# Optimization experiments

Measured on AMD Instinct MI355X. Metric: run time of the kernel, lower is better.

Reference implementation:

```python
import jax, jax.numpy as jnp
import numpy as np

B, S, DIM, H = 2, 2048, 1024, 16
HD = DIM // H  # 64


def setup_inputs() -> dict:
    key = jax.random.key(0)
    ks = jax.random.split(key, 7)
    sc = 1.0 / np.sqrt(DIM)
    gammas = jnp.asarray(1.0 - 2.0 ** (-5.0 - np.arange(H)), jnp.float32)  # RetNet per-head decay
    return {
        "q": jax.random.normal(ks[0], (B, S, DIM), jnp.float32),
        "k": jax.random.normal(ks[1], (B, S, DIM), jnp.float32),
        "v": jax.random.normal(ks[2], (B, S, DIM), jnp.float32),
        "W_in": jax.random.normal(ks[3], (DIM, DIM), jnp.float32) * sc,
        "b_in": jnp.zeros((DIM,), jnp.float32),
        "W_gate": jax.random.normal(ks[4], (DIM, DIM), jnp.float32) * sc,
        "b_gate": jnp.zeros((DIM,), jnp.float32),
        "W_out": jax.random.normal(ks[5], (DIM, DIM), jnp.float32) * sc,
        "b_out": jnp.zeros((DIM,), jnp.float32),
        "gammas": gammas,
    }


def _mamba(x, W_in, b_in, W_gate, b_gate, W_out, b_out):
    # Gated linear recurrence: h_t = a_t * h_{t-1} + u_t  (selective-scan style)
    u = x @ W_in + b_in          # [B,S,D]
    a = jax.nn.sigmoid(x @ W_gate + b_gate)  # [B,S,D] data-dependent decay gate

    def combine(c1, c2):
        a1, u1 = c1
        a2, u2 = c2
        return (a1 * a2, a2 * u1 + u2)

    _, h = jax.lax.associative_scan(combine, (a, u), axis=1)  # parallel scan over S
    return h @ W_out + b_out  # residual=False, dropout=0.0


def _retention(q, k, v, gammas):
    # Per-head decay-masked attention: out = ((Q K^T / sqrt(hd)) * D) V,
    # D[h,n,m] = gamma_h^(n-m) for n>=m else 0 (causal decay kernel).
    def split(x):
        return x.reshape(B, S, H, HD).transpose(0, 2, 1, 3)  # [B,H,S,HD]

    qh, kh, vh = split(q), split(k), split(v)
    idx = jnp.arange(S)
    diff = idx[:, None] - idx[None, :]                        # [S,S]
    expnt = jnp.maximum(diff, 0).astype(jnp.float32)
    D = jnp.where(diff >= 0, gammas[:, None, None] ** expnt, 0.0)  # [H,S,S]
    scores = jnp.einsum("bhnd,bhmd->bhnm", qh, kh) / np.sqrt(HD)
    out = jnp.einsum("bhnm,bhmd->bhnd", scores * D[None], vh)
    return out.transpose(0, 2, 1, 3).reshape(B, S, DIM)


def reference(q, k, v, W_in, b_in, W_gate, b_gate, W_out, b_out, gammas):
    q_proj = _mamba(q, W_in, b_in, W_gate, b_gate, W_out, b_out)
    return _retention(q_proj, k, v, gammas)
```

## Files before the change

kernel.cpp:

```cpp
#include <hip/hip_runtime.h>
#include <math.h>

#define B_  2
#define S_  2048
#define D_  1024
#define H_  16
#define HD_ 64
#define M_  (B_*S_)

typedef unsigned short ushort_t;
typedef unsigned int   uint_t;
typedef __attribute__((ext_vector_type(8))) short bf16x8;
typedef __attribute__((ext_vector_type(4))) float f32x4;

__device__ __forceinline__ ushort_t f2bf(float f) {
    uint_t u = __builtin_bit_cast(uint_t, f);
    u += 0x7FFFu + ((u >> 16) & 1u);
    return (ushort_t)(u >> 16);
}
__device__ __forceinline__ float bf2f(ushort_t h) {
    uint_t u = (uint_t)h << 16;
    return __builtin_bit_cast(float, u);
}
__device__ __forceinline__ uint_t pkt(float lo, float hi) {
    return __builtin_amdgcn_perm(__builtin_bit_cast(uint_t, hi),
                                 __builtin_bit_cast(uint_t, lo), 0x07060302u);
}
__device__ __forceinline__ void dma16(const ushort_t* g, ushort_t* l) {
    __builtin_amdgcn_global_load_lds(
        (const __attribute__((address_space(1))) uint_t*)g,
        (__attribute__((address_space(3))) uint_t*)l, 16, 0, 0);
}
__device__ __forceinline__ bf16x8 fragr(const ushort_t* base, int row, int chunk) {
    return *(const bf16x8*)&base[row * 64 + (((chunk ^ (row & 7)) << 3))];
}

__global__ __launch_bounds__(256)
void prep(const float* __restrict__ W0, const float* __restrict__ W1,
          const float* __restrict__ W2, ushort_t* __restrict__ T0,
          ushort_t* __restrict__ T1, ushort_t* __restrict__ T2,
          const float* __restrict__ X, ushort_t* __restrict__ Y) {
    const int bx = blockIdx.x;
    if (bx >= 3072) {
        const int i = ((bx - 3072) * 256 + threadIdx.x) * 4;
        float4 x = *(const float4*)(X + i);
        *(ushort4*)(Y + i) = make_ushort4(f2bf(x.x), f2bf(x.y), f2bf(x.z), f2bf(x.w));
        return;
    }
    __shared__ float T[32][36];
    const int z = bx >> 10;
    const float*  W  = (z == 0) ? W0 : (z == 1) ? W1 : W2;
    ushort_t*     WT = (z == 0) ? T0 : (z == 1) ? T1 : T2;
    const int kt = bx & 31, nt = (bx >> 5) & 31;
    const int t = threadIdx.x;
    const int rr = t >> 3, cc = (t & 7) * 4;
    float4 w4 = *(const float4*)(W + (size_t)(kt * 32 + rr) * D_ + nt * 32 + cc);
    T[rr][cc + 0] = w4.x; T[rr][cc + 1] = w4.y; T[rr][cc + 2] = w4.z; T[rr][cc + 3] = w4.w;
    __syncthreads();
    ushort_t o[4];
    #pragma unroll
    for (int j = 0; j < 4; ++j) o[j] = f2bf(T[cc + j][rr]);
    *(ushort4*)(WT + (size_t)(nt * 32 + rr) * D_ + kt * 32 + cc) =
        make_ushort4(o[0], o[1], o[2], o[3]);
}

__global__ __launch_bounds__(256)
void gemm_dual_kv(const ushort_t* __restrict__ A, const ushort_t* __restrict__ BTi,
                  const ushort_t* __restrict__ BTg, const float* __restrict__ bi,
                  const float* __restrict__ bg, float* __restrict__ Hloc,
                  ushort_t* __restrict__ Pp, float* __restrict__ cA,
                  float* __restrict__ cU,
                  const float* __restrict__ K, const float* __restrict__ V,
                  const float* __restrict__ gammas, ushort_t* __restrict__ Kb,
                  ushort_t* __restrict__ VT, float* __restrict__ Gg) {
    __shared__ ushort_t smem[32768];
    const int tid = threadIdx.x;
    const int w = tid >> 6, lane = tid & 63, quad = lane >> 4, l15 = lane & 15;

    if (blockIdx.x >= 512) {
        ushort_t* Tv = smem;
        ushort_t* Tk = smem + 64 * 72;
        const int idx = blockIdx.x - 512;
        const int mt = idx & 31, h = (idx >> 5) & 15, b = idx >> 9;
        const int m0 = mt * 64;
        const int r = tid >> 2, c0 = (tid & 3) * 16;
        const float lg = log2f(gammas[h]);
        const float gm = exp2f(-(float)r * lg);
        {
            const float* src = K + ((size_t)(b * S_ + m0 + r)) * D_ + h * HD_ + c0;
            ushort_t kb[16];
            #pragma unroll
            for (int j4 = 0; j4 < 4; ++j4) {
                float4 x = *(const float4*)(src + j4 * 4);
                kb[j4 * 4 + 0] = f2bf(x.x); kb[j4 * 4 + 1] = f2bf(x.y);
                kb[j4 * 4 + 2] = f2bf(x.z); kb[j4 * 4 + 3] = f2bf(x.w);
            }
            ushort_t* dst = Kb + ((size_t)(b * S_ + m0 + r)) * D_ + h * HD_ + c0;
            *(uint4*)(dst + 0) = *(const uint4*)&kb[0];
            *(uint4*)(dst + 8) = *(const uint4*)&kb[8];
            #pragma unroll
            for (int j = 0; j < 16; ++j) Tk[(c0 + j) * 72 + r] = kb[j];
        }
        {
            const float* src = V + ((size_t)(b * S_ + m0 + r)) * D_ + h * HD_ + c0;
            #pragma unroll
            for (int j4 = 0; j4 < 4; ++j4) {
                float4 x = *(const float4*)(src + j4 * 4);
                Tv[(c0 + j4 * 4 + 0) * 72 + r] = f2bf(x.x * gm);
                Tv[(c0 + j4 * 4 + 1) * 72 + r] = f2bf(x.y * gm);
                Tv[(c0 + j4 * 4 + 2) * 72 + r] = f2bf(x.z * gm);
                Tv[(c0 + j4 * 4 + 3) * 72 + r] = f2bf(x.w * gm);
            }
        }
        __syncthreads();
        {
            ushort_t* dst = VT + ((size_t)((b * H_ + h) * HD_ + r)) * S_ + m0 + c0;
            *(uint4*)(dst + 0) = *(const uint4*)&Tv[r * 72 + c0 + 0];
            *(uint4*)(dst + 8) = *(const uint4*)&Tv[r * 72 + c0 + 8];
        }
        bf16x8 af0 = *(const bf16x8*)&Tv[(w * 16 + l15) * 72 + quad * 8];
        bf16x8 af1 = *(const bf16x8*)&Tv[(w * 16 + l15) * 72 + 32 + quad * 8];
        float* gout = Gg + ((size_t)((b * H_ + h) * 32 + mt)) * 4096;
        #pragma unroll
        for (int kt2 = 0; kt2 < 4; ++kt2) {
            bf16x8 bf0 = *(const bf16x8*)&Tk[(kt2 * 16 + l15) * 72 + quad * 8];
            bf16x8 bf1 = *(const bf16x8*)&Tk[(kt2 * 16 + l15) * 72 + 32 + quad * 8];
            f32x4 g = {};
            g = __builtin_amdgcn_mfma_f32_16x16x32_bf16(af0, bf0, g, 0, 0, 0);
            g = __builtin_amdgcn_mfma_f32_16x16x32_bf16(af1, bf1, g, 0, 0, 0);
            #pragma unroll
            for (int reg = 0; reg < 4; ++reg)
                gout[(w * 16 + quad * 4 + reg) * 64 + kt2 * 16 + l15] = g[reg];
        }
        return;
    }

    const int swz = (blockIdx.x & 7) * 64 + (blockIdx.x >> 3);
    const int n0 = (swz & 15) * 64, m0 = (swz >> 4) * 128;
    const int wr = (w >> 1) * 64, wc = (w & 1) * 32;
    const int l8 = lane & 7, lr8 = lane >> 3;

    f32x4 acc_i[4][2] = {};
    f32x4 acc_g[4][2] = {};

    auto stage = [&](int k0, int bufo) {
        #pragma unroll
        for (int t = 0; t < 4; ++t) {
            const int row = w * 32 + t * 8 + lr8;
            const int gc = ((l8 ^ (row & 7)) << 3);
            dma16(A + (size_t)(m0 + row) * D_ + k0 + gc, &smem[bufo + row * 64 + l8 * 8]);
        }
        #pragma unroll
        for (int t = 0; t < 2; ++t) {
            const int row = w * 16 + t * 8 + lr8;
            const int gc = ((l8 ^ (row & 7)) << 3);
            dma16(BTi + (size_t)(n0 + row) * D_ + k0 + gc, &smem[bufo + 8192 + row * 64 + l8 * 8]);
            dma16(BTg + (size_t)(n0 + row) * D_ + k0 + gc, &smem[bufo + 12288 + row * 64 + l8 * 8]);
        }
    };

    stage(0, 0);
    __syncthreads();
    for (int t = 0; t < 16; ++t) {
        const int bufo = (t & 1) * 16384;
        if (t < 15) stage((t + 1) * 64, 16384 - bufo);
        const ushort_t* As = smem + bufo;
        const ushort_t* Bi = smem + bufo + 8192;
        const ushort_t* Bg = smem + bufo + 12288;
        #pragma unroll
        for (int kk = 0; kk < 2; ++kk) {
            bf16x8 af[4], bfi[2], bfg[2];
            #pragma unroll
            for (int i = 0; i < 4; ++i)
                af[i] = fragr(As, wr + 16 * i + l15, kk * 4 + quad);
            #pragma unroll
            for (int j = 0; j < 2; ++j) {
                bfi[j] = fragr(Bi, wc + 16 * j + l15, kk * 4 + quad);
                bfg[j] = fragr(Bg, wc + 16 * j + l15, kk * 4 + quad);
            }
            #pragma unroll
            for (int i = 0; i < 4; ++i)
                #pragma unroll
                for (int j = 0; j < 2; ++j) {
                    acc_i[i][j] = __builtin_amdgcn_mfma_f32_16x16x32_bf16(
                        af[i], bfi[j], acc_i[i][j], 0, 0, 0);
                    acc_g[i][j] = __builtin_amdgcn_mfma_f32_16x16x32_bf16(
                        af[i], bfg[j], acc_g[i][j], 0, 0, 0);
                }
        }
        __syncthreads();
    }

    ushort_t* Us = smem;
    ushort_t* Gu = smem + 8448;
    #pragma unroll
    for (int j = 0; j < 2; ++j) {
        const int n = wc + 16 * j + l15;
        const float bbi = bi[n0 + n], bbg = bg[n0 + n];
        #pragma unroll
        for (int i = 0; i < 4; ++i) {
            #pragma unroll
            for (int r = 0; r < 4; ++r) {
                const int m = wr + 16 * i + quad * 4 + r;
                Us[m * 66 + n] = f2bf(acc_i[i][j][r] + bbi);
                float g = 1.0f / (1.0f + __expf(-(acc_g[i][j][r] + bbg)));
                Gu[m * 66 + n] = (ushort_t)__float2uint_rn(g * 65535.0f);
            }
        }
    }
    __syncthreads();

    const int nl = tid & 63, c = tid >> 6;
    const int gmb = m0 + c * 32;
    const size_t gbase = (size_t)gmb * D_ + n0 + nl;
    float Aa = 1.0f, hh = 0.0f;
    #pragma unroll 4
    for (int j = 0; j < 32; ++j) {
        const float g = (float)Gu[(c * 32 + j) * 66 + nl] * (1.0f / 65535.0f);
        const float u = bf2f(Us[(c * 32 + j) * 66 + nl]);
        Aa *= g;
        hh = fmaf(g, hh, u);
        Pp[gbase + (size_t)j * D_] = f2bf(Aa);
        Hloc[gbase + (size_t)j * D_] = hh;
    }
    const int bb = gmb >> 11;
    const int ch = (gmb & 2047) >> 5;
    const int ci = ((bb * 64 + ch) << 10) + n0 + nl;
    cA[ci] = Aa;
    cU[ci] = hh;
}

__global__ __launch_bounds__(256)
void mid_scan(const float* __restrict__ Gg, const float* __restrict__ gammas,
              ushort_t* __restrict__ Sb, const float* __restrict__ cA,
              const float* __restrict__ cU, float* __restrict__ cIn) {
    const int bi = blockIdx.x;
    if (bi < 128) {
        const int sl = bi & 3, h = (bi >> 2) & 15, b = bi >> 6;
        const float g64 = exp2f(64.0f * log2f(gammas[h]));
        const int r = threadIdx.x >> 4;
        const int cb = (threadIdx.x & 15) * 4;
        const size_t base = ((size_t)((b * H_ + h) * 32)) * 4096 + (sl * 16 + r) * 64 + cb;
        float4 S = make_float4(0.f, 0.f, 0.f, 0.f);
        for (int c = 0; c < 32; ++c) {
            ushort4 sb;
            sb.x = f2bf(S.x); sb.y = f2bf(S.y); sb.z = f2bf(S.z); sb.w = f2bf(S.w);
            *(ushort4*)(Sb + base + (size_t)c * 4096) = sb;
            float4 G = *(const float4*)(Gg + base + (size_t)c * 4096);
            S.x = g64 * (S.x + G.x); S.y = g64 * (S.y + G.y);
            S.z = g64 * (S.z + G.z); S.w = g64 * (S.w + G.w);
        }
        return;
    }
    const int t = (bi - 128) * 256 + threadIdx.x;
    const int d = t & 1023, b = t >> 10;
    float h = 0.0f;
    for (int c0 = 0; c0 < 64; c0 += 16) {
        float Av[16], Uv[16];
        #pragma unroll
        for (int j = 0; j < 16; ++j) {
            const int idx = ((b * 64 + c0 + j) << 10) + d;
            Av[j] = cA[idx]; Uv[j] = cU[idx];
        }
        #pragma unroll
        for (int j = 0; j < 16; ++j) {
            cIn[((b * 64 + c0 + j) << 10) + d] = h;
            h = fmaf(Av[j], h, Uv[j]);
        }
    }
}

__global__ __launch_bounds__(256)
void scan_fix(const float* __restrict__ Hloc, const ushort_t* __restrict__ Pp,
              const float* __restrict__ cIn, ushort_t* __restrict__ hout) {
    const int i = (blockIdx.x * 256 + threadIdx.x) * 4;
    const int m = i >> 10, d = i & 1023;
    const int b = m >> 11, ch = (m & 2047) >> 5;
    float4 hl = *(const float4*)(Hloc + i);
    ushort4 p4 = *(const ushort4*)(Pp + i);
    float4 ci = *(const float4*)(cIn + ((b * 64 + ch) << 10) + d);
    ushort4 o;
    o.x = f2bf(fmaf(ci.x, bf2f(p4.x), hl.x));
    o.y = f2bf(fmaf(ci.y, bf2f(p4.y), hl.y));
    o.z = f2bf(fmaf(ci.z, bf2f(p4.z), hl.z));
    o.w = f2bf(fmaf(ci.w, bf2f(p4.w), hl.w));
    *(ushort4*)(hout + i) = o;
}

__global__ __launch_bounds__(256)
void gemm_out_ret(const ushort_t* __restrict__ A, const ushort_t* __restrict__ BT,
                  const float* __restrict__ bias, const ushort_t* __restrict__ Kb,
                  const ushort_t* __restrict__ VT, const ushort_t* __restrict__ Sb,
                  const float* __restrict__ gammas, float* __restrict__ Out) {
    __shared__ ushort_t smem[24576];
    const int tid = threadIdx.x;
    const int flat = blockIdx.x + (blockIdx.y << 4);
    const int swz = (flat & 7) * 64 + (flat >> 3);
    const int h = swz & 15;
    const int n0 = h * 64, m0 = (swz >> 4) * 128;
    const int w = tid >> 6, lane = tid & 63, quad = lane >> 4, l15 = lane & 15;
    const int wr = (w >> 1) * 64, wc = (w & 1) * 32;
    const int l8 = lane & 7, lr8 = lane >> 3;

    ushort_t* Qs = smem;
    ushort_t* Ks = smem + 8192;
    ushort_t* Vt = smem + 12288;
    ushort_t* Ss = smem + 16384;
    ushort_t* Ps = smem + 20480;

    auto stageK = [&](int sc) {
        const int mrow = m0 + sc * 64;
        const size_t bS2 = (size_t)(mrow >> 11) * S_;
        const int s0r = mrow & 2047;
        #pragma unroll
        for (int t2 = 0; t2 < 2; ++t2) {
            const int row = w * 16 + t2 * 8 + lr8;
            const int gc = ((l8 ^ (row & 7)) << 3);
            dma16(Kb + (bS2 + s0r + row) * D_ + h * HD_ + gc, &Ks[row * 64 + l8 * 8]);
        }
    };
    auto stageV = [&](int sc) {
        const int mrow = m0 + sc * 64;
        const size_t vrow0 = (size_t)(((mrow >> 11) * H_ + h) * HD_);
        const int s0r = mrow & 2047;
        #pragma unroll
        for (int t2 = 0; t2 < 2; ++t2) {
            const int row = w * 16 + t2 * 8 + lr8;
            const int gc = ((l8 ^ (row & 7)) << 3);
            dma16(VT + (vrow0 + row) * S_ + s0r + gc, &Vt[row * 64 + l8 * 8]);
        }
    };
    auto stageS = [&](int sc) {
        const int mrow = m0 + sc * 64;
        const size_t sbase = ((size_t)(((mrow >> 11) * H_ + h) * 32 + ((mrow & 2047) >> 6))) * 4096;
        #pragma unroll
        for (int t2 = 0; t2 < 2; ++t2) {
            const int row = w * 16 + t2 * 8 + lr8;
            const int gc = ((l8 ^ (row & 7)) << 3);
            dma16(Sb + sbase + (size_t)row * 64 + gc, &Ss[row * 64 + l8 * 8]);
        }
    };

    f32x4 acc[4][2] = {};

    auto stage = [&](int k0, int bufo) {
        #pragma unroll
        for (int t = 0; t < 4; ++t) {
            const int row = w * 32 + t * 8 + lr8;
            const int gc = ((l8 ^ (row & 7)) << 3);
            dma16(A + (size_t)(m0 + row) * D_ + k0 + gc, &smem[bufo + row * 64 + l8 * 8]);
        }
        #pragma unroll
        for (int t = 0; t < 2; ++t) {
            const int row = w * 16 + t * 8 + lr8;
            const int gc = ((l8 ^ (row & 7)) << 3);
            dma16(BT + (size_t)(n0 + row) * D_ + k0 + gc, &smem[bufo + 8192 + row * 64 + l8 * 8]);
        }
    };

    stage(0, 0);
    __syncthreads();
    for (int t = 0; t < 16; ++t) {
        const int bufo = (t & 1) * 12288;
        if (t < 15) stage((t + 1) * 64, 12288 - bufo);
        if (t == 15) stageK(0);
        const ushort_t* As = smem + bufo;
        const ushort_t* Bs = smem + bufo + 8192;
        #pragma unroll
        for (int kk = 0; kk < 2; ++kk) {
            bf16x8 af[4], bf[2];
            #pragma unroll
            for (int i = 0; i < 4; ++i)
                af[i] = fragr(As, wr + 16 * i + l15, kk * 4 + quad);
            #pragma unroll
            for (int j = 0; j < 2; ++j)
                bf[j] = fragr(Bs, wc + 16 * j + l15, kk * 4 + quad);
            #pragma unroll
            for (int i = 0; i < 4; ++i)
                #pragma unroll
                for (int j = 0; j < 2; ++j)
                    acc[i][j] = __builtin_amdgcn_mfma_f32_16x16x32_bf16(
                        af[i], bf[j], acc[i][j], 0, 0, 0);
        }
        __syncthreads();
    }

    stageV(0);
    stageS(0);

    #pragma unroll
    for (int j = 0; j < 2; ++j) {
        const int n = wc + 16 * j + l15;
        const float bb = bias[n0 + n];
        #pragma unroll
        for (int i = 0; i < 4; ++i)
            #pragma unroll
            for (int r = 0; r < 4; ++r) {
                const int m = wr + 16 * i + quad * 4 + r;
                Qs[m * 64 + (((n >> 3) ^ (m & 7)) << 3) + (n & 7)] =
                    f2bf((acc[i][j][r] + bb) * 0.125f);
            }
    }

    const float lg = log2f(gammas[h]);
    const int nl = w * 16 + l15;

    for (int sc = 0; sc < 2; ++sc) {
        __syncthreads();
        const int mrow = m0 + sc * 64;
        const size_t bS = (size_t)(mrow >> 11) * S_;
        const int s0 = mrow & 2047;
        const ushort_t* Qsub = Qs + sc * 64 * 64;

        bf16x8 qf0 = fragr(Qsub, nl, quad);
        bf16x8 qf1 = fragr(Qsub, nl, 4 + quad);

        f32x4 o[4] = {};
        #pragma unroll
        for (int ct = 0; ct < 4; ++ct) {
            bf16x8 sf0 = fragr(Ss, ct * 16 + l15, quad);
            bf16x8 sf1 = fragr(Ss, ct * 16 + l15, 4 + quad);
            o[ct] = __builtin_amdgcn_mfma_f32_16x16x32_bf16(sf0, qf0, o[ct], 0, 0, 0);
            o[ct] = __builtin_amdgcn_mfma_f32_16x16x32_bf16(sf1, qf1, o[ct], 0, 0, 0);
        }
        uint2 pw[4];
        #pragma unroll
        for (int mt2 = 0; mt2 < 4; ++mt2) {
            bf16x8 kf0 = fragr(Ks, mt2 * 16 + l15, quad);
            bf16x8 kf1 = fragr(Ks, mt2 * 16 + l15, 4 + quad);
            f32x4 s = {};
            s = __builtin_amdgcn_mfma_f32_16x16x32_bf16(kf0, qf0, s, 0, 0, 0);
            s = __builtin_amdgcn_mfma_f32_16x16x32_bf16(kf1, qf1, s, 0, 0, 0);
            const int mbase = mt2 * 16 + quad * 4;
            #pragma unroll
            for (int r = 0; r < 4; ++r)
                if (nl < mbase + r) s[r] = 0.0f;
            pw[mt2].x = pkt(s[0], s[1]); pw[mt2].y = pkt(s[2], s[3]);
        }
        __syncthreads();
        if (sc == 0) { stageK(1); stageS(1); }
        #pragma unroll
        for (int mt2 = 0; mt2 < 4; ++mt2) {
            const int mbase = mt2 * 16 + quad * 4;
            const int chunk = mbase >> 3;
            *(uint2*)&Ps[nl * 64 + ((chunk ^ (nl & 7)) << 3) + (mbase & 7)] = pw[mt2];
        }
        bf16x8 pf0 = fragr(Ps, nl, quad);
        bf16x8 pf1 = fragr(Ps, nl, 4 + quad);
        #pragma unroll
        for (int ct = 0; ct < 4; ++ct) {
            bf16x8 vf0 = fragr(Vt, ct * 16 + l15, quad);
            bf16x8 vf1 = fragr(Vt, ct * 16 + l15, 4 + quad);
            o[ct] = __builtin_amdgcn_mfma_f32_16x16x32_bf16(vf0, pf0, o[ct], 0, 0, 0);
            o[ct] = __builtin_amdgcn_mfma_f32_16x16x32_bf16(vf1, pf1, o[ct], 0, 0, 0);
        }

        const float esc = exp2f((float)nl * lg);
        const size_t ob = (bS + s0 + nl) * D_ + h * HD_;
        #pragma unroll
        for (int ct = 0; ct < 4; ++ct) {
            f32x4 t = o[ct] * esc;
            *(f32x4*)(Out + ob + ct * 16 + quad * 4) = t;
        }
        __syncthreads();
        if (sc == 0) stageV(1);
    }
}

extern "C" void kernel_launch(void* const* d_in, const int* in_sizes, int n_in,
                              void* d_out, int out_size, void* d_ws, size_t ws_size,
                              hipStream_t stream) {
    const float* q      = (const float*)d_in[0];
    const float* k      = (const float*)d_in[1];
    const float* v      = (const float*)d_in[2];
    const float* W_in   = (const float*)d_in[3];
    const float* b_in   = (const float*)d_in[4];
    const float* W_gate = (const float*)d_in[5];
    const float* b_gate = (const float*)d_in[6];
    const float* W_out  = (const float*)d_in[7];
    const float* b_out  = (const float*)d_in[8];
    const float* gammas = (const float*)d_in[9];
    float* out = (float*)d_out;

    char* ws = (char*)d_ws;
    const size_t MB = 1024 * 1024;
    float*    Hloc    = (float*)(ws);
    ushort_t* Pp      = (ushort_t*)(ws + 16 * MB);
    ushort_t* h_bf    = (ushort_t*)(ws + 24 * MB);
    ushort_t* q_bf    = (ushort_t*)(ws + 32 * MB);
    ushort_t* WT_in   = (ushort_t*)(ws + 40 * MB);
    ushort_t* WT_gate = (ushort_t*)(ws + 42 * MB);
    ushort_t* WT_out  = (ushort_t*)(ws + 44 * MB);
    float*    cA      = (float*)(ws + 46 * MB);
    float*    cU      = (float*)(ws + 46 * MB + 512 * 1024);
    float*    cIn     = (float*)(ws + 47 * MB);
    ushort_t* k_bf    = (ushort_t*)(ws + 48 * MB);
    ushort_t* VT      = (ushort_t*)(ws + 56 * MB);
    float*    Gg      = (float*)(ws + 64 * MB);
    ushort_t* Sb      = (ushort_t*)(ws + 80 * MB);

    prep<<<3072 + (M_ * D_) / (256 * 4), 256, 0, stream>>>(
        W_in, W_gate, W_out, WT_in, WT_gate, WT_out, q, q_bf);

    gemm_dual_kv<<<512 + 1024, 256, 0, stream>>>(
        q_bf, WT_in, WT_gate, b_in, b_gate, Hloc, Pp, cA, cU,
        k, v, gammas, k_bf, VT, Gg);

    mid_scan<<<136, 256, 0, stream>>>(Gg, gammas, Sb, cA, cU, cIn);
    scan_fix<<<(M_ * D_) / 1024, 256, 0, stream>>>(Hloc, Pp, cIn, h_bf);

    gemm_out_ret<<<dim3(H_, M_ / 128), 256, 0, stream>>>(
        h_bf, WT_out, b_out, k_bf, VT, Sb, gammas, out);
}
```

Baseline: 174.5 us.

## Fuse mid-scan, scan fixup and output GEMM into one cooperative kernel

Replaces three separate launches (mid_scan, scan_fix, gemm_out_ret) with a single cooperative kernel of 512 blocks that uses grid-wide syncs between phases. The scan fixup is redistributed so each block processes eight strided chunks. This removes two kernel launch boundaries and their drain and fill gaps, at the cost of grid.sync overhead and a requirement that all 512 blocks be co-resident. Occupancy for the GEMM phase may now be limited by the cooperative launch constraints.

```diff
diff --git a/kernel.cpp b/kernel.cpp
--- a/kernel.cpp
+++ b/kernel.cpp
@@ -1,5 +1,8 @@
 #include <hip/hip_runtime.h>
+#include <hip/hip_cooperative_groups.h>
 #include <math.h>
+
+namespace cg = cooperative_groups;
 
 #define B_  2
 #define S_  2048
@@ -231,15 +234,24 @@
 }
 
 __global__ __launch_bounds__(256)
-void mid_scan(const float* __restrict__ Gg, const float* __restrict__ gammas,
-              ushort_t* __restrict__ Sb, const float* __restrict__ cA,
-              const float* __restrict__ cU, float* __restrict__ cIn) {
+void tail_fused(const float* __restrict__ Gg, const float* __restrict__ gammas,
+                ushort_t* __restrict__ Sb, const float* __restrict__ cA,
+                const float* __restrict__ cU, float* __restrict__ cIn,
+                const float* __restrict__ Hloc, const ushort_t* __restrict__ Pp,
+                ushort_t* __restrict__ hout,
+                const ushort_t* __restrict__ BT, const float* __restrict__ bias,
+                const ushort_t* __restrict__ Kb, const ushort_t* __restrict__ VT,
+                float* __restrict__ Out) {
+    __shared__ ushort_t smem[24576];
+    cg::grid_group grid = cg::this_grid();
     const int bi = blockIdx.x;
+    const int tid = threadIdx.x;
+
     if (bi < 128) {
         const int sl = bi & 3, h = (bi >> 2) & 15, b = bi >> 6;
         const float g64 = exp2f(64.0f * log2f(gammas[h]));
-        const int r = threadIdx.x >> 4;
-        const int cb = (threadIdx.x & 15) * 4;
+        const int r = tid >> 4;
+        const int cb = (tid & 15) * 4;
         const size_t base = ((size_t)((b * H_ + h) * 32)) * 4096 + (sl * 16 + r) * 64 + cb;
         float4 S = make_float4(0.f, 0.f, 0.f, 0.f);
         for (int c = 0; c < 32; ++c) {
@@ -250,51 +262,47 @@
             S.x = g64 * (S.x + G.x); S.y = g64 * (S.y + G.y);
             S.z = g64 * (S.z + G.z); S.w = g64 * (S.w + G.w);
         }
-        return;
-    }
-    const int t = (bi - 128) * 256 + threadIdx.x;
-    const int d = t & 1023, b = t >> 10;
-    float h = 0.0f;
-    for (int c0 = 0; c0 < 64; c0 += 16) {
-        float Av[16], Uv[16];
-        #pragma unroll
-        for (int j = 0; j < 16; ++j) {
-            const int idx = ((b * 64 + c0 + j) << 10) + d;
-            Av[j] = cA[idx]; Uv[j] = cU[idx];
-        }
-        #pragma unroll
-        for (int j = 0; j < 16; ++j) {
-            cIn[((b * 64 + c0 + j) << 10) + d] = h;
-            h = fmaf(Av[j], h, Uv[j]);
-        }
-    }
-}
-
-__global__ __launch_bounds__(256)
-void scan_fix(const float* __restrict__ Hloc, const ushort_t* __restrict__ Pp,
-              const float* __restrict__ cIn, ushort_t* __restrict__ hout) {
-    const int i = (blockIdx.x * 256 + threadIdx.x) * 4;
-    const int m = i >> 10, d = i & 1023;
-    const int b = m >> 11, ch = (m & 2047) >> 5;
-    float4 hl = *(const float4*)(Hloc + i);
-    ushort4 p4 = *(const ushort4*)(Pp + i);
-    float4 ci = *(const float4*)(cIn + ((b * 64 + ch) << 10) + d);
-    ushort4 o;
-    o.x = f2bf(fmaf(ci.x, bf2f(p4.x), hl.x));
-    o.y = f2bf(fmaf(ci.y, bf2f(p4.y), hl.y));
-    o.z = f2bf(fmaf(ci.z, bf2f(p4.z), hl.z));
-    o.w = f2bf(fmaf(ci.w, bf2f(p4.w), hl.w));
-    *(ushort4*)(hout + i) = o;
-}
-
-__global__ __launch_bounds__(256)
-void gemm_out_ret(const ushort_t* __restrict__ A, const ushort_t* __restrict__ BT,
-                  const float* __restrict__ bias, const ushort_t* __restrict__ Kb,
-                  const ushort_t* __restrict__ VT, const ushort_t* __restrict__ Sb,
-                  const float* __restrict__ gammas, float* __restrict__ Out) {
-    __shared__ ushort_t smem[24576];
-    const int tid = threadIdx.x;
-    const int flat = blockIdx.x + (blockIdx.y << 4);
+    } else if (bi < 136) {
+        const int t = (bi - 128) * 256 + tid;
+        const int d = t & 1023, b = t >> 10;
+        float h = 0.0f;
+        for (int c0 = 0; c0 < 64; c0 += 16) {
+            float Av[16], Uv[16];
+            #pragma unroll
+            for (int j = 0; j < 16; ++j) {
+                const int idx = ((b * 64 + c0 + j) << 10) + d;
+                Av[j] = cA[idx]; Uv[j] = cU[idx];
+            }
+            #pragma unroll
+            for (int j = 0; j < 16; ++j) {
+                cIn[((b * 64 + c0 + j) << 10) + d] = h;
+                h = fmaf(Av[j], h, Uv[j]);
+            }
+        }
+    }
+    __threadfence();
+    grid.sync();
+
+    #pragma unroll
+    for (int it = 0; it < 8; ++it) {
+        const int i = ((it * 512 + bi) * 256 + tid) * 4;
+        const int m = i >> 10, d = i & 1023;
+        const int b = m >> 11, ch = (m & 2047) >> 5;
+        float4 hl = *(const float4*)(Hloc + i);
+        ushort4 p4 = *(const ushort4*)(Pp + i);
+        float4 ci = *(const float4*)(cIn + ((b * 64 + ch) << 10) + d);
+        ushort4 o;
+        o.x = f2bf(fmaf(ci.x, bf2f(p4.x), hl.x));
+        o.y = f2bf(fmaf(ci.y, bf2f(p4.y), hl.y));
+        o.z = f2bf(fmaf(ci.z, bf2f(p4.z), hl.z));
+        o.w = f2bf(fmaf(ci.w, bf2f(p4.w), hl.w));
+        *(ushort4*)(hout + i) = o;
+    }
+    __threadfence();
+    grid.sync();
+
+    const ushort_t* A = hout;
+    const int flat = bi;
     const int swz = (flat & 7) * 64 + (flat >> 3);
     const int h = swz & 15;
     const int n0 = h * 64, m0 = (swz >> 4) * 128;
@@ -506,9 +514,16 @@
         q_bf, WT_in, WT_gate, b_in, b_gate, Hloc, Pp, cA, cU,
         k, v, gammas, k_bf, VT, Gg);
 
-    mid_scan<<<136, 256, 0, stream>>>(Gg, gammas, Sb, cA, cU, cIn);
-    scan_fix<<<(M_ * D_) / 1024, 256, 0, stream>>>(Hloc, Pp, cIn, h_bf);
-
-    gemm_out_ret<<<dim3(H_, M_ / 128), 256, 0, stream>>>(
-        h_bf, WT_out, b_out, k_bf, VT, Sb, gammas, out);
-}
+    const float* Gg_c = Gg; const float* cA_c = cA; const float* cU_c = cU;
+    const float* Hloc_c = Hloc; const ushort_t* Pp_c = Pp;
+    const ushort_t* WT_out_c = WT_out; const ushort_t* k_bf_c = k_bf;
+    const ushort_t* VT_c = VT;
+    void* args[] = {
+        (void*)&Gg_c, (void*)&gammas, (void*)&Sb, (void*)&cA_c, (void*)&cU_c,
+        (void*)&cIn, (void*)&Hloc_c, (void*)&Pp_c, (void*)&h_bf,
+        (void*)&WT_out_c, (void*)&b_out, (void*)&k_bf_c, (void*)&VT_c,
+        (void*)&out
+    };
+    hipLaunchCooperativeKernel((const void*)tail_fused, dim3(512), dim3(256),
+                               args, 0, stream);
+}
```

After: 390.8 us. 124% more time.

## Move K/V prep into prep kernel and overlap retention state scan with dual GEMM

Applied to the files above, without the earlier changes.

The K/V bf16 conversion and per-chunk KV Gram computation move out of the dual GEMM kernel into the prep kernel. The retention chunk-state scan, which depends only on Gg, now runs as extra blocks inside the dual GEMM kernel. This lets the state scan overlap with the GEMM, and the carry scan becomes a small standalone kernel. The cost is a larger prep grid with shared memory raised for every block, and the serial state-scan blocks may end up on the GEMM's critical tail.

```diff
diff --git a/kernel.cpp b/kernel.cpp
--- a/kernel.cpp
+++ b/kernel.cpp
@@ -39,50 +39,20 @@
 void prep(const float* __restrict__ W0, const float* __restrict__ W1,
           const float* __restrict__ W2, ushort_t* __restrict__ T0,
           ushort_t* __restrict__ T1, ushort_t* __restrict__ T2,
-          const float* __restrict__ X, ushort_t* __restrict__ Y) {
+          const float* __restrict__ X, ushort_t* __restrict__ Y,
+          const float* __restrict__ K, const float* __restrict__ V,
+          const float* __restrict__ gammas, ushort_t* __restrict__ Kb,
+          ushort_t* __restrict__ VT, float* __restrict__ Gg) {
+    __shared__ ushort_t pbuf[2 * 64 * 72];
     const int bx = blockIdx.x;
-    if (bx >= 3072) {
-        const int i = ((bx - 3072) * 256 + threadIdx.x) * 4;
-        float4 x = *(const float4*)(X + i);
-        *(ushort4*)(Y + i) = make_ushort4(f2bf(x.x), f2bf(x.y), f2bf(x.z), f2bf(x.w));
-        return;
-    }
-    __shared__ float T[32][36];
-    const int z = bx >> 10;
-    const float*  W  = (z == 0) ? W0 : (z == 1) ? W1 : W2;
-    ushort_t*     WT = (z == 0) ? T0 : (z == 1) ? T1 : T2;
-    const int kt = bx & 31, nt = (bx >> 5) & 31;
-    const int t = threadIdx.x;
-    const int rr = t >> 3, cc = (t & 7) * 4;
-    float4 w4 = *(const float4*)(W + (size_t)(kt * 32 + rr) * D_ + nt * 32 + cc);
-    T[rr][cc + 0] = w4.x; T[rr][cc + 1] = w4.y; T[rr][cc + 2] = w4.z; T[rr][cc + 3] = w4.w;
-    __syncthreads();
-    ushort_t o[4];
-    #pragma unroll
-    for (int j = 0; j < 4; ++j) o[j] = f2bf(T[cc + j][rr]);
-    *(ushort4*)(WT + (size_t)(nt * 32 + rr) * D_ + kt * 32 + cc) =
-        make_ushort4(o[0], o[1], o[2], o[3]);
-}
-
-__global__ __launch_bounds__(256)
-void gemm_dual_kv(const ushort_t* __restrict__ A, const ushort_t* __restrict__ BTi,
-                  const ushort_t* __restrict__ BTg, const float* __restrict__ bi,
-                  const float* __restrict__ bg, float* __restrict__ Hloc,
-                  ushort_t* __restrict__ Pp, float* __restrict__ cA,
-                  float* __restrict__ cU,
-                  const float* __restrict__ K, const float* __restrict__ V,
-                  const float* __restrict__ gammas, ushort_t* __restrict__ Kb,
-                  ushort_t* __restrict__ VT, float* __restrict__ Gg) {
-    __shared__ ushort_t smem[32768];
     const int tid = threadIdx.x;
-    const int w = tid >> 6, lane = tid & 63, quad = lane >> 4, l15 = lane & 15;
-
-    if (blockIdx.x >= 512) {
-        ushort_t* Tv = smem;
-        ushort_t* Tk = smem + 64 * 72;
-        const int idx = blockIdx.x - 512;
-        const int mt = idx & 31, h = (idx >> 5) & 15, b = idx >> 9;
+
+    if (bx < 1024) {
+        ushort_t* Tv = pbuf;
+        ushort_t* Tk = pbuf + 64 * 72;
+        const int mt = bx & 31, h = (bx >> 5) & 15, b = bx >> 9;
         const int m0 = mt * 64;
+        const int w = tid >> 6, lane = tid & 63, quad = lane >> 4, l15 = lane & 15;
         const int r = tid >> 2, c0 = (tid & 3) * 16;
         const float lg = log2f(gammas[h]);
         const float gm = exp2f(-(float)r * lg);
@@ -135,6 +105,62 @@
         return;
     }
 
+    if (bx >= 4096) {
+        const int i = ((bx - 4096) * 256 + tid) * 4;
+        float4 x = *(const float4*)(X + i);
+        *(ushort4*)(Y + i) = make_ushort4(f2bf(x.x), f2bf(x.y), f2bf(x.z), f2bf(x.w));
+        return;
+    }
+
+    float* T = (float*)pbuf;
+    const int wz = bx - 1024;
+    const int z = wz >> 10;
+    const float*  W  = (z == 0) ? W0 : (z == 1) ? W1 : W2;
+    ushort_t*     WT = (z == 0) ? T0 : (z == 1) ? T1 : T2;
+    const int kt = wz & 31, nt = (wz >> 5) & 31;
+    const int rr = tid >> 3, cc = (tid & 7) * 4;
+    float4 w4 = *(const float4*)(W + (size_t)(kt * 32 + rr) * D_ + nt * 32 + cc);
+    T[rr * 36 + cc + 0] = w4.x; T[rr * 36 + cc + 1] = w4.y;
+    T[rr * 36 + cc + 2] = w4.z; T[rr * 36 + cc + 3] = w4.w;
+    __syncthreads();
+    ushort_t o[4];
+    #pragma unroll
+    for (int j = 0; j < 4; ++j) o[j] = f2bf(T[(cc + j) * 36 + rr]);
+    *(ushort4*)(WT + (size_t)(nt * 32 + rr) * D_ + kt * 32 + cc) =
+        make_ushort4(o[0], o[1], o[2], o[3]);
+}
+
+__global__ __launch_bounds__(256)
+void gemm_dual_sc(const ushort_t* __restrict__ A, const ushort_t* __restrict__ BTi,
+                  const ushort_t* __restrict__ BTg, const float* __restrict__ bi,
+                  const float* __restrict__ bg, float* __restrict__ Hloc,
+                  ushort_t* __restrict__ Pp, float* __restrict__ cA,
+                  float* __restrict__ cU,
+                  const float* __restrict__ Gg, const float* __restrict__ gammas,
+                  ushort_t* __restrict__ Sb) {
+    __shared__ ushort_t smem[32768];
+    const int tid = threadIdx.x;
+
+    if (blockIdx.x >= 512) {
+        const int bi2 = blockIdx.x - 512;
+        const int sl = bi2 & 3, h = (bi2 >> 2) & 15, b = bi2 >> 6;
+        const float g64 = exp2f(64.0f * log2f(gammas[h]));
+        const int r = tid >> 4;
+        const int cb = (tid & 15) * 4;
+        const size_t base = ((size_t)((b * H_ + h) * 32)) * 4096 + (sl * 16 + r) * 64 + cb;
+        float4 S = make_float4(0.f, 0.f, 0.f, 0.f);
+        for (int c = 0; c < 32; ++c) {
+            ushort4 sb;
+            sb.x = f2bf(S.x); sb.y = f2bf(S.y); sb.z = f2bf(S.z); sb.w = f2bf(S.w);
+            *(ushort4*)(Sb + base + (size_t)c * 4096) = sb;
+            float4 G = *(const float4*)(Gg + base + (size_t)c * 4096);
+            S.x = g64 * (S.x + G.x); S.y = g64 * (S.y + G.y);
+            S.z = g64 * (S.z + G.z); S.w = g64 * (S.w + G.w);
+        }
+        return;
+    }
+
+    const int w = tid >> 6, lane = tid & 63, quad = lane >> 4, l15 = lane & 15;
     const int swz = (blockIdx.x & 7) * 64 + (blockIdx.x >> 3);
     const int n0 = (swz & 15) * 64, m0 = (swz >> 4) * 128;
     const int wr = (w >> 1) * 64, wc = (w & 1) * 32;
@@ -231,28 +257,9 @@
 }
 
 __global__ __launch_bounds__(256)
-void mid_scan(const float* __restrict__ Gg, const float* __restrict__ gammas,
-              ushort_t* __restrict__ Sb, const float* __restrict__ cA,
-              const float* __restrict__ cU, float* __restrict__ cIn) {
-    const int bi = blockIdx.x;
-    if (bi < 128) {
-        const int sl = bi & 3, h = (bi >> 2) & 15, b = bi >> 6;
-        const float g64 = exp2f(64.0f * log2f(gammas[h]));
-        const int r = threadIdx.x >> 4;
-        const int cb = (threadIdx.x & 15) * 4;
-        const size_t base = ((size_t)((b * H_ + h) * 32)) * 4096 + (sl * 16 + r) * 64 + cb;
-        float4 S = make_float4(0.f, 0.f, 0.f, 0.f);
-        for (int c = 0; c < 32; ++c) {
-            ushort4 sb;
-            sb.x = f2bf(S.x); sb.y = f2bf(S.y); sb.z = f2bf(S.z); sb.w = f2bf(S.w);
-            *(ushort4*)(Sb + base + (size_t)c * 4096) = sb;
-            float4 G = *(const float4*)(Gg + base + (size_t)c * 4096);
-            S.x = g64 * (S.x + G.x); S.y = g64 * (S.y + G.y);
-            S.z = g64 * (S.z + G.z); S.w = g64 * (S.w + G.w);
-        }
-        return;
-    }
-    const int t = (bi - 128) * 256 + threadIdx.x;
+void carry_scan(const float* __restrict__ cA, const float* __restrict__ cU,
+                float* __restrict__ cIn) {
+    const int t = blockIdx.x * 256 + threadIdx.x;
     const int d = t & 1023, b = t >> 10;
     float h = 0.0f;
     for (int c0 = 0; c0 < 64; c0 += 16) {
@@ -499,14 +506,16 @@
     float*    Gg      = (float*)(ws + 64 * MB);
     ushort_t* Sb      = (ushort_t*)(ws + 80 * MB);
 
-    prep<<<3072 + (M_ * D_) / (256 * 4), 256, 0, stream>>>(
-        W_in, W_gate, W_out, WT_in, WT_gate, WT_out, q, q_bf);
-
-    gemm_dual_kv<<<512 + 1024, 256, 0, stream>>>(
+    prep<<<8192, 256, 0, stream>>>(
+        W_in, W_gate, W_out, WT_in, WT_gate, WT_out, q, q_bf,
+        k, v, gammas, k_bf, VT, Gg);
+
+    gemm_dual_sc<<<640, 256, 0, stream>>>(
         q_bf, WT_in, WT_gate, b_in, b_gate, Hloc, Pp, cA, cU,
-        k, v, gammas, k_bf, VT, Gg);
-
-    mid_scan<<<136, 256, 0, stream>>>(Gg, gammas, Sb, cA, cU, cIn);
+        Gg, gammas, Sb);
+
+    carry_scan<<<8, 256, 0, stream>>>(cA, cU, cIn);
+
     scan_fix<<<(M_ * D_) / 1024, 256, 0, stream>>>(Hloc, Pp, cIn, h_bf);
 
     gemm_out_ret<<<dim3(H_, M_ / 128), 256, 0, stream>>>(
```

After: 176.3 us. About the same (+1.0%).
